# Kernel optimization log

Hardware: AMD Instinct MI355X
Metric: run time of the kernel (lower is better)

The kernel has to match this reference:

```python
import jax, jax.numpy as jnp
import numpy as np

NUM_HEADS = 8
NUM_CLS = 1
WINDOW = 4          # one-sided window radius
DILATION = 2
THETA = 10000.0
COORD_HIGH = 100000.0


def _rotate_half(t):
    # [..., x1, x2, ...] -> [..., -x2, x1, ...]
    x1 = t[..., 0::2]
    x2 = t[..., 1::2]
    return jnp.stack([-x2, x1], axis=-1).reshape(t.shape)


def _rope2d(t, coords):
    # t: (B, H, L, D), coords: (B, L, 2)
    head_dim = t.shape[-1]
    half = head_dim // 2
    inv_freq = 1.0 / (THETA ** (jnp.arange(0, half, 2, dtype=jnp.float32) / half))  # (half//2,)
    xy = coords.astype(jnp.float32) / COORD_HIGH                                    # (B, L, 2)
    fx = xy[..., 0][..., None] * inv_freq                                           # (B, L, half//2)
    fy = xy[..., 1][..., None] * inv_freq
    fx = jnp.repeat(fx, 2, axis=-1)                                                 # (B, L, half)
    fy = jnp.repeat(fy, 2, axis=-1)
    freqs = jnp.concatenate([fx, fy], axis=-1)                                      # (B, L, D)
    cos = jnp.cos(freqs)[:, None]                                                   # (B, 1, L, D)
    sin = jnp.sin(freqs)[:, None]
    return t * cos + _rotate_half(t) * sin


def setup_inputs() -> dict:
    key = jax.random.key(0)
    k1, k2, k3, k4 = jax.random.split(key, 4)
    B, L, E = 2, 8192, 512
    S = NUM_CLS + L
    x = jax.random.normal(k1, (B, S, E), dtype=jnp.float32)
    coords = jax.random.randint(k2, (B, L, 2), 0, 100000, dtype=jnp.int32)
    w_qkv = jax.random.normal(k3, (3 * E, E), dtype=jnp.float32) * 0.02
    b_qkv = jnp.zeros((3 * E,), dtype=jnp.float32)
    w_out = jax.random.normal(k4, (E, E), dtype=jnp.float32) * 0.02
    b_out = jnp.zeros((E,), dtype=jnp.float32)
    return {"x": x, "coords": coords, "w_qkv": w_qkv, "b_qkv": b_qkv,
            "w_out": w_out, "b_out": b_out}


def reference(x, coords, w_qkv, b_qkv, w_out, b_out):
    B, S, E = x.shape
    H = NUM_HEADS
    D = E // H
    L = S - NUM_CLS
    scale = 1.0 / np.sqrt(D).astype(np.float32)

    qkv = x @ w_qkv.T + b_qkv                                  # (B, S, 3E)
    qkv = qkv.reshape(B, S, 3, H, D).transpose(2, 0, 3, 1, 4)  # (3, B, H, S, D)
    q, k, v = qkv[0], qkv[1], qkv[2]

    # 2D RoPE on patch tokens only
    q = jnp.concatenate([q[:, :, :NUM_CLS], _rope2d(q[:, :, NUM_CLS:], coords)], axis=2)
    k = jnp.concatenate([k[:, :, :NUM_CLS], _rope2d(k[:, :, NUM_CLS:], coords)], axis=2)

    # ---- global CLS queries attend to all tokens ----
    s_cls = jnp.einsum('bhqd,bhkd->bhqk', q[:, :, :NUM_CLS], k) * scale
    cls_out = jnp.einsum('bhqk,bhkd->bhqd', jax.nn.softmax(s_cls, axis=-1), v)

    # ---- patch queries: CLS keys + dilated local window ----
    q_p = q[:, :, NUM_CLS:]
    k_p, v_p = k[:, :, NUM_CLS:], v[:, :, NUM_CLS:]
    k_cls, v_cls = k[:, :, :NUM_CLS], v[:, :, :NUM_CLS]

    pad = WINDOW * DILATION
    W = 2 * WINDOW + 1
    kp = jnp.pad(k_p, ((0, 0), (0, 0), (pad, pad), (0, 0)))
    vp = jnp.pad(v_p, ((0, 0), (0, 0), (pad, pad), (0, 0)))

    pos = jnp.arange(L)
    offsets = jnp.arange(W) * DILATION
    gidx = pos[:, None] + offsets[None, :]                     # (L, W), indices into padded seq
    kw = jnp.take(kp, gidx, axis=2)                            # (B, H, L, W, D)
    vw = jnp.take(vp, gidx, axis=2)

    win_pos = (jnp.arange(W) - WINDOW) * DILATION
    in_bounds = (pos[:, None] + win_pos >= 0) & (pos[:, None] + win_pos < L)  # (L, W)

    s_win = jnp.einsum('bhld,bhlwd->bhlw', q_p, kw) * scale
    s_win = jnp.where(in_bounds, s_win, -jnp.inf)
    s_c = jnp.einsum('bhld,bhcd->bhlc', q_p, k_cls) * scale
    attn = jax.nn.softmax(jnp.concatenate([s_c, s_win], axis=-1), axis=-1)  # (B,H,L,C+W)

    patch_out = (jnp.einsum('bhlc,bhcd->bhld', attn[..., :NUM_CLS], v_cls)
                 + jnp.einsum('bhlw,bhlwd->bhld', attn[..., NUM_CLS:], vw))

    out = jnp.concatenate([cls_out, patch_out], axis=2)        # (B, H, S, D)
    out = out.transpose(0, 2, 1, 3).reshape(B, S, E)
    return out @ w_out.T + b_out
```

## Files before the change

kernel.cpp:

```cpp
#include <hip/hip_runtime.h>
#include <math.h>

#define B_ 2
#define S_ 8193
#define L_ 8192
#define E_ 512
#define H_ 8
#define D_ 64
#define QKV_COLS 1536
#define SCALE 0.125f
#define M_ROWS 16386
#define M_PAD 16512

typedef unsigned short u16;
typedef __attribute__((ext_vector_type(8))) short bf16x8;
typedef __attribute__((ext_vector_type(8))) unsigned short u16x8;
typedef __attribute__((ext_vector_type(4))) float f32x4;

__device__ __forceinline__ u16 f2bf(float f) {
    unsigned u = __float_as_uint(f);
    unsigned r = (u + 0x7fffu + ((u >> 16) & 1u)) >> 16;
    return (u16)r;
}
__device__ __forceinline__ float bf2f(u16 h) {
    return __uint_as_float((unsigned)h << 16);
}

__device__ __forceinline__ void gload_lds16(const void* g, void* l) {
    __builtin_amdgcn_global_load_lds(
        (const __attribute__((address_space(1))) void*)g,
        (__attribute__((address_space(3))) void*)l, 16, 0, 0);
}

#define WAITV8() asm volatile("s_waitcnt vmcnt(8)" ::: "memory")
#define WAITV4() asm volatile("s_waitcnt vmcnt(4)" ::: "memory")
#define WAITV0() asm volatile("s_waitcnt vmcnt(0)" ::: "memory")
#define LGKM0()  asm volatile("s_waitcnt lgkmcnt(0)" ::: "memory")
#define BAR()    __builtin_amdgcn_s_barrier()

#define PREP_W1 (QKV_COLS * E_ / 4)
#define PREP_W2 (E_ * E_ / 4)
#define PREP_W3 (B_ * L_ * 32)
#define PREP_W4 ((M_PAD - M_ROWS) * E_ / 8)
#define PREP_TOTAL (PREP_W1 + PREP_W2 + PREP_W3 + PREP_W4)

__global__ __launch_bounds__(256) void prep_kernel(
    const float* __restrict__ w_qkv, const float* __restrict__ w_out,
    const int* __restrict__ coords,
    u16* __restrict__ wqb, u16* __restrict__ wob,
    float2* __restrict__ tab, u16* __restrict__ attnb)
{
    long i = (long)blockIdx.x * 256 + threadIdx.x;
    if (i < PREP_W1) {
        const float4 v = *(const float4*)(w_qkv + i * 4);
        ushort4 o = { f2bf(v.x), f2bf(v.y), f2bf(v.z), f2bf(v.w) };
        *(ushort4*)(wqb + i * 4) = o;
        return;
    }
    i -= PREP_W1;
    if (i < PREP_W2) {
        const float4 v = *(const float4*)(w_out + i * 4);
        ushort4 o = { f2bf(v.x), f2bf(v.y), f2bf(v.z), f2bf(v.w) };
        *(ushort4*)(wob + i * 4) = o;
        return;
    }
    i -= PREP_W2;
    if (i < PREP_W3) {
        const int p2 = (int)i & 31;
        const int bl = (int)i >> 5;
        const float coord = (float)coords[(size_t)bl * 2 + (p2 >> 4)] * 1e-5f;
        const float inv = exp2f(-0.83048202372184f * (float)(p2 & 15));
        float sn, cs;
        __sincosf(coord * inv, &sn, &cs);
        tab[i] = make_float2(cs, sn);
        return;
    }
    i -= PREP_W3;
    if (i < PREP_W4) {
        u16x8 z = {};
        *(u16x8*)(attnb + (size_t)M_ROWS * E_ + i * 8) = z;
    }
}

__global__ __launch_bounds__(512, 4) void gemm_qkv_fused(
    const float* __restrict__ X, const u16* __restrict__ W,
    const float* __restrict__ bias, u16* __restrict__ C,
    const float2* __restrict__ tab, int M, int N, int K)
{
    __shared__ __align__(16) u16 smem[16384];

    const int nwg = gridDim.x * gridDim.y;
    const int orig = blockIdx.y * gridDim.x + blockIdx.x;
    const int qq = nwg >> 3, rr = nwg & 7;
    const int xcd = orig & 7, off = orig >> 3;
    const int wgid = (xcd < rr ? xcd * (qq + 1) : rr * (qq + 1) + (xcd - rr) * qq) + off;
    const int m0 = (wgid / gridDim.x) * 128;
    const int n0 = (wgid % gridDim.x) * 128;

    const int tid  = threadIdx.x;
    const int wid  = tid >> 6;
    const int lane = tid & 63;
    const int wm = (wid >> 2) * 64;
    const int wn = (wid & 3) * 32;
    const int fr = lane & 15;
    const int fq = lane >> 4;

    const int r0 = tid >> 3;
    const int c8 = tid & 7;
    const int aoff0 = r0 * 32 + (((c8 >> 1) ^ (r0 & 3)) * 8) + (c8 & 1) * 4;

    const int wrow = tid >> 2;
    const int wch  = (tid & 3) ^ (wrow & 3);

    float4 ra[2];
    f32x4 acc[4][2] = {};

    #define ALOAD(k0)                                                           \
        do {                                                                    \
            _Pragma("unroll")                                                   \
            for (int i = 0; i < 2; ++i) {                                       \
                const int gm = m0 + r0 + 64 * i;                                \
                ra[i] = (gm < M)                                                \
                    ? *(const float4*)(X + (size_t)gm * K + (k0) + c8 * 4)      \
                    : make_float4(0.f, 0.f, 0.f, 0.f);                          \
            }                                                                   \
        } while (0)

    #define ADSW(buf)                                                           \
        do {                                                                    \
            u16* as_ = smem + (buf) * 4096;                                     \
            _Pragma("unroll")                                                   \
            for (int i = 0; i < 2; ++i) {                                       \
                ushort4 o;                                                      \
                o.x = f2bf(ra[i].x); o.y = f2bf(ra[i].y);                       \
                o.z = f2bf(ra[i].z); o.w = f2bf(ra[i].w);                       \
                *(ushort4*)(as_ + aoff0 + 2048 * i) = o;                        \
            }                                                                   \
        } while (0)

    #define WSTAGE(buf, k0)                                                     \
        gload_lds16(W + (size_t)(n0 + wrow) * K + (k0) + wch * 8,               \
                    smem + 8192 + (buf) * 4096 + wid * 512)

    #define COMPUTE(buf)                                                         \
        do {                                                                     \
            const u16* as_ = smem + (buf) * 4096;                                \
            const u16* bs_ = smem + 8192 + (buf) * 4096;                         \
            bf16x8 a[4], b[2];                                                   \
            _Pragma("unroll")                                                    \
            for (int mi = 0; mi < 4; ++mi) {                                     \
                const int r_ = wm + mi * 16 + fr;                                \
                a[mi] = *(const bf16x8*)(as_ + r_ * 32 + ((fq ^ (r_ & 3)) * 8)); \
            }                                                                    \
            _Pragma("unroll")                                                    \
            for (int ni = 0; ni < 2; ++ni) {                                     \
                const int r_ = wn + ni * 16 + fr;                                \
                b[ni] = *(const bf16x8*)(bs_ + r_ * 32 + ((fq ^ (r_ & 3)) * 8)); \
            }                                                                    \
            _Pragma("unroll")                                                    \
            for (int mi = 0; mi < 4; ++mi)                                       \
                _Pragma("unroll")                                                \
                for (int ni = 0; ni < 2; ++ni)                                   \
                    acc[mi][ni] = __builtin_amdgcn_mfma_f32_16x16x32_bf16(       \
                        a[mi], b[ni], acc[mi][ni], 0, 0, 0);                     \
        } while (0)

    const int nt = K / 32;

    ALOAD(0); WSTAGE(0, 0);
    WAITV0();
    ADSW(0);
    ALOAD(32); WSTAGE(1, 32);
    LGKM0(); BAR();

    for (int t = 0; t < nt; ++t) {
        COMPUTE(t & 1);
        if (t + 1 < nt) {
            WAITV0();
            ADSW((t + 1) & 1);
            if (t + 2 < nt) ALOAD((t + 2) * 32);
            LGKM0(); BAR();
            if (t + 2 < nt) WSTAGE(t & 1, (t + 2) * 32);
        }
    }

    #undef ALOAD
    #undef ADSW
    #undef WSTAGE
    #undef COMPUTE

    __syncthreads();

    u16* st = smem;
    const bool rope_blk = (n0 < 2 * E_);
    #pragma unroll
    for (int mi = 0; mi < 4; ++mi) {
        #pragma unroll
        for (int j = 0; j < 4; ++j) {
            const int row = wm + mi * 16 + fq * 4 + j;
            const int gm = m0 + row;
            int b = 0, s = gm;
            if (gm >= S_) { b = 1; s = gm - S_; }
            const bool rot = rope_blk && (gm < M) && (s > 0);
            const float2* trow = tab + ((size_t)(b * L_ + (s - 1)) << 5);
            #pragma unroll
            for (int ni = 0; ni < 2; ++ni) {
                const int col = wn + ni * 16 + fr;
                const int gn = n0 + col;
                float v = acc[mi][ni][j] + bias[gn];
                const float partner = __shfl_xor(v, 1, 64);
                if (rot) {
                    const float2 tt = trow[(gn & 63) >> 1];
                    v = (gn & 1) ? (v * tt.x + partner * tt.y)
                                 : (v * tt.x - partner * tt.y);
                }
                st[row * 128 + col] = f2bf(v);
            }
        }
    }
    __syncthreads();
    #pragma unroll
    for (int i = 0; i < 4; ++i) {
        const int slot = i * 512 + tid;
        const int row = slot >> 4;
        const int coff = (slot & 15) * 8;
        const int gm = m0 + row;
        if (gm < M)
            *(u16x8*)(C + (size_t)gm * N + n0 + coff) =
                *(const u16x8*)(st + row * 128 + coff);
    }
}

__global__ __launch_bounds__(256) void gemm_out_128(
    const u16* __restrict__ A, const u16* __restrict__ W,
    const float* __restrict__ bias, float* __restrict__ C,
    int M, int N, int K)
{
    __shared__ __align__(16) u16 smem[32768];

    const int nwg = gridDim.x * gridDim.y;
    const int orig = blockIdx.y * gridDim.x + blockIdx.x;
    const int qq = nwg >> 3, rr = nwg & 7;
    const int xcd = orig & 7, off = orig >> 3;
    const int wgid = (xcd < rr ? xcd * (qq + 1) : rr * (qq + 1) + (xcd - rr) * qq) + off;
    const int m0 = (wgid / gridDim.x) * 128;
    const int n0 = (wgid % gridDim.x) * 128;

    const int tid  = threadIdx.x;
    const int wid  = tid >> 6;
    const int lane = tid & 63;
    const int wm = (wid >> 1) * 64;
    const int wn = (wid & 1) * 64;

    const int srow = lane >> 2;
    const int scol = ((lane & 3) ^ ((lane >> 3) & 3)) * 8;
    const int fr = lane & 15;
    const int fq = lane >> 4;
    const int sfq = (fq ^ ((fr >> 1) & 3)) * 8;

    const int c0 = wid * 2, c1 = wid * 2 + 1;
    const u16* ga0 = A + (size_t)(m0 + c0 * 16 + srow) * K + scol;
    const u16* ga1 = A + (size_t)(m0 + c1 * 16 + srow) * K + scol;
    const u16* gb0 = W + (size_t)(n0 + c0 * 16 + srow) * K + scol;
    const u16* gb1 = W + (size_t)(n0 + c1 * 16 + srow) * K + scol;
    const int la0 = c0 * 16 * 32, la1 = c1 * 16 * 32;

    f32x4 acc[4][4] = {};

    #define STAGE(bi, k0)                                       \
        do {                                                    \
            u16* as_ = smem + (bi) * 4096;                      \
            u16* bs_ = smem + 16384 + (bi) * 4096;              \
            gload_lds16(ga0 + (k0), as_ + la0);                 \
            gload_lds16(ga1 + (k0), as_ + la1);                 \
            gload_lds16(gb0 + (k0), bs_ + la0);                 \
            gload_lds16(gb1 + (k0), bs_ + la1);                 \
        } while (0)

    #define COMPUTE(bi)                                                          \
        do {                                                                     \
            const u16* as_ = smem + (bi) * 4096;                                 \
            const u16* bs_ = smem + 16384 + (bi) * 4096;                         \
            bf16x8 a[4], b[4];                                                   \
            _Pragma("unroll")                                                    \
            for (int mi = 0; mi < 4; ++mi)                                       \
                a[mi] = *(const bf16x8*)(as_ + (wm + mi * 16 + fr) * 32 + sfq);  \
            _Pragma("unroll")                                                    \
            for (int ni = 0; ni < 4; ++ni)                                       \
                b[ni] = *(const bf16x8*)(bs_ + (wn + ni * 16 + fr) * 32 + sfq);  \
            _Pragma("unroll")                                                    \
            for (int mi = 0; mi < 4; ++mi)                                       \
                _Pragma("unroll")                                                \
                for (int ni = 0; ni < 4; ++ni)                                   \
                    acc[mi][ni] = __builtin_amdgcn_mfma_f32_16x16x32_bf16(       \
                        a[mi], b[ni], acc[mi][ni], 0, 0, 0);                     \
        } while (0)

    const int nt = K / 32;

    STAGE(0, 0);
    STAGE(1, 32);
    STAGE(2, 64);

    int t = 0;
    for (; t <= nt - 4; ++t) {
        WAITV8(); BAR();
        COMPUTE(t & 3);
        STAGE((t + 3) & 3, (t + 3) * 32);
    }
    WAITV8(); BAR(); COMPUTE(t & 3); ++t;
    WAITV4(); BAR(); COMPUTE(t & 3); ++t;
    WAITV0(); BAR(); COMPUTE(t & 3);

    #undef STAGE
    #undef COMPUTE

    __syncthreads();

    float* stf = (float*)smem;
    #pragma unroll
    for (int mi = 0; mi < 4; ++mi)
        #pragma unroll
        for (int j = 0; j < 4; ++j) {
            const int r = wm + mi * 16 + fq * 4 + j;
            #pragma unroll
            for (int ni = 0; ni < 4; ++ni) {
                const int c = wn + ni * 16 + fr;
                stf[r * 128 + c] = acc[mi][ni][j] + bias[n0 + c];
            }
        }
    __syncthreads();
    #pragma unroll
    for (int i = 0; i < 16; ++i) {
        const int ch = i * 256 + tid;
        const int row = ch >> 5;
        const int coff = (ch & 31) * 4;
        const int gm = m0 + row;
        if (gm < M)
            *(float4*)(C + (size_t)gm * N + n0 + coff) =
                *(const float4*)(stf + row * 128 + coff);
    }
}

#define NCHUNK 64
#define CLS_ROWS 129
#define CLS_BLOCKS (B_ * H_ * NCHUNK)
#define PQT 256
#define PATCH_BLOCKS (B_ * H_ * (L_ / PQT))

__global__ __launch_bounds__(256) void attn_fused(
    const u16* __restrict__ qkvb, float* __restrict__ part,
    u16* __restrict__ attnb)
{
    __shared__ __align__(16) u16 sbuf[272 * 64];
    __shared__ float kcvc[128];
    __shared__ float sm4[4], sl4[4];

    const int blk = blockIdx.x;

    if (blk < CLS_BLOCKS) {
        const int bh = blk >> 6, ch = blk & 63;
        const int b = bh >> 3, h = bh & 7;
        const int wid = threadIdx.x >> 6, lane = threadIdx.x & 63;
        const size_t base = (size_t)b * S_ * QKV_COLS;

        const float q = bf2f(qkvb[base + h * D_ + lane]);

        const int lo = ch * CLS_ROWS;
        const int hi = (lo + CLS_ROWS < S_) ? lo + CLS_ROWS : S_;

        float m = -1e30f, lsum = 0.f, acc = 0.f;
        for (int j = lo + wid; j < hi; j += 4) {
            const size_t roff = base + (size_t)j * QKV_COLS;
            float t = q * bf2f(qkvb[roff + E_ + h * D_ + lane]);
            #pragma unroll
            for (int o = 32; o; o >>= 1) t += __shfl_xor(t, o, 64);
            t *= SCALE;
            const float mn = fmaxf(m, t);
            const float corr = __expf(m - mn);
            const float p = __expf(t - mn);
            lsum = lsum * corr + p;
            acc = acc * corr + p * bf2f(qkvb[roff + 2 * E_ + h * D_ + lane]);
            m = mn;
        }

        float* sacc = (float*)sbuf;
        if (lane == 0) { sm4[wid] = m; sl4[wid] = lsum; }
        sacc[wid * 64 + lane] = acc;
        __syncthreads();
        if (wid == 0) {
            const float gm = fmaxf(fmaxf(sm4[0], sm4[1]), fmaxf(sm4[2], sm4[3]));
            float gl = 0.f, ga = 0.f;
            #pragma unroll
            for (int w = 0; w < 4; ++w) {
                const float c = __expf(sm4[w] - gm);
                gl += sl4[w] * c;
                ga += sacc[w * 64 + lane] * c;
            }
            float* pp = part + ((size_t)bh * NCHUNK + ch) * 66;
            if (lane == 0) { pp[0] = gm; pp[1] = gl; }
            pp[2 + lane] = ga;
        }
        return;
    }

    const int pblk = blk - CLS_BLOCKS;
    const int qt = pblk & 31;
    const int h = (pblk >> 5) & 7;
    const int b = pblk >> 8;
    const int l0 = qt * PQT;
    const size_t base = (size_t)b * S_ * QKV_COLS;
    const int hoff = h * D_;

    u16* kv = sbuf;
    float* kc = kcvc;
    float* vc = kcvc + 64;

    const int t = threadIdx.x;

    if (t < 64) kc[t] = bf2f(qkvb[base + E_ + hoff + t]);
    else if (t < 128) vc[t - 64] = bf2f(qkvb[base + 2 * E_ + hoff + (t - 64)]);

    #pragma unroll
    for (int i = 0; i < 9; ++i) {
        const int s = i * 256 + t;
        if (s < 272 * 8) {
            const int r = s >> 3, c = s & 7;
            const int lg = l0 - 8 + r;
            u16x8 v = {};
            if (lg >= 0 && lg < L_)
                v = *(const u16x8*)(qkvb + base + (size_t)(1 + lg) * QKV_COLS + E_ + hoff + c * 8);
            *(u16x8*)(kv + r * 64 + ((c ^ (r & 7)) * 8)) = v;
        }
    }
    __syncthreads();

    const int l = l0 + t;
    const size_t qrow = base + (size_t)(1 + l) * QKV_COLS + hoff;

    float s[10];
    #pragma unroll
    for (int w = 0; w < 10; ++w) s[w] = 0.f;

    #pragma unroll
    for (int c = 0; c < 8; ++c) {
        const u16x8 qv = *(const u16x8*)(qkvb + qrow + c * 8);
        float qf[8];
        #pragma unroll
        for (int i = 0; i < 8; ++i) qf[i] = bf2f(qv[i]);
        #pragma unroll
        for (int i = 0; i < 8; ++i) s[0] += qf[i] * kc[c * 8 + i];
        #pragma unroll
        for (int w = 0; w < 9; ++w) {
            const int kr = t + 2 * w;
            const u16x8 kk = *(const u16x8*)(kv + kr * 64 + ((c ^ (kr & 7)) * 8));
            #pragma unroll
            for (int i = 0; i < 8; ++i) s[1 + w] += qf[i] * bf2f(kk[i]);
        }
    }

    s[0] *= SCALE;
    #pragma unroll
    for (int w = 0; w < 9; ++w) {
        const int lp = l + 2 * w - 8;
        s[1 + w] = (lp >= 0 && lp < L_) ? s[1 + w] * SCALE : -1e30f;
    }
    float m = s[0];
    #pragma unroll
    for (int w = 1; w < 10; ++w) m = fmaxf(m, s[w]);
    float sum = 0.f;
    #pragma unroll
    for (int w = 0; w < 10; ++w) { s[w] = __expf(s[w] - m); sum += s[w]; }
    const float rsum = 1.0f / sum;

    __syncthreads();
    #pragma unroll
    for (int i = 0; i < 9; ++i) {
        const int sl = i * 256 + t;
        if (sl < 272 * 8) {
            const int r = sl >> 3, c = sl & 7;
            const int lg = l0 - 8 + r;
            u16x8 v = {};
            if (lg >= 0 && lg < L_)
                v = *(const u16x8*)(qkvb + base + (size_t)(1 + lg) * QKV_COLS + 2 * E_ + hoff + c * 8);
            *(u16x8*)(kv + r * 64 + ((c ^ (r & 7)) * 8)) = v;
        }
    }
    __syncthreads();

    const size_t orow = (size_t)(b * S_ + 1 + l) * E_ + hoff;
    #pragma unroll
    for (int c = 0; c < 8; ++c) {
        float acc[8];
        #pragma unroll
        for (int i = 0; i < 8; ++i) acc[i] = s[0] * vc[c * 8 + i];
        #pragma unroll
        for (int w = 0; w < 9; ++w) {
            const int vr = t + 2 * w;
            const u16x8 vv = *(const u16x8*)(kv + vr * 64 + ((c ^ (vr & 7)) * 8));
            #pragma unroll
            for (int i = 0; i < 8; ++i) acc[i] += s[1 + w] * bf2f(vv[i]);
        }
        u16x8 o;
        #pragma unroll
        for (int i = 0; i < 8; ++i) o[i] = f2bf(acc[i] * rsum);
        *(u16x8*)(attnb + orow + c * 8) = o;
    }
}

__global__ __launch_bounds__(64) void cls_attn_stage2(
    const float* __restrict__ part, u16* __restrict__ attnb)
{
    const int bh = blockIdx.x;
    const int lane = threadIdx.x;
    const int b = bh >> 3, h = bh & 7;
    float gm = -1e30f;
    for (int c = 0; c < NCHUNK; ++c)
        gm = fmaxf(gm, part[((size_t)bh * NCHUNK + c) * 66]);
    float gl = 0.f, ga = 0.f;
    for (int c = 0; c < NCHUNK; ++c) {
        const float* pp = part + ((size_t)bh * NCHUNK + c) * 66;
        const float w = __expf(pp[0] - gm);
        gl += pp[1] * w;
        ga += pp[2 + lane] * w;
    }
    attnb[(size_t)(b * S_) * E_ + h * D_ + lane] = f2bf(ga / gl);
}

extern "C" void kernel_launch(void* const* d_in, const int* in_sizes, int n_in,
                              void* d_out, int out_size, void* d_ws, size_t ws_size,
                              hipStream_t stream)
{
    const float* x      = (const float*)d_in[0];
    const int*   coords = (const int*)  d_in[1];
    const float* w_qkv  = (const float*)d_in[2];
    const float* b_qkv  = (const float*)d_in[3];
    const float* w_out  = (const float*)d_in[4];
    const float* b_out  = (const float*)d_in[5];
    float* out = (float*)d_out;

    u16*   qkvb  = (u16*)d_ws;
    u16*   attnb = qkvb + (size_t)M_ROWS * QKV_COLS;
    u16*   wqb   = attnb + (size_t)M_PAD * E_;
    u16*   wob   = wqb + (size_t)QKV_COLS * E_;
    float* part  = (float*)(wob + (size_t)E_ * E_);
    float2* tab  = (float2*)(part + (size_t)16 * NCHUNK * 66);

    prep_kernel<<<(PREP_TOTAL + 255) / 256, 256, 0, stream>>>(
        w_qkv, w_out, coords, wqb, wob, tab, attnb);

    {
        dim3 grid(QKV_COLS / 128, M_PAD / 128);
        gemm_qkv_fused<<<grid, 512, 0, stream>>>(
            x, wqb, b_qkv, qkvb, tab, M_ROWS, QKV_COLS, E_);
    }

    attn_fused<<<CLS_BLOCKS + PATCH_BLOCKS, 256, 0, stream>>>(qkvb, part, attnb);

    cls_attn_stage2<<<B_ * H_, 64, 0, stream>>>(part, attnb);

    {
        dim3 grid(E_ / 128, M_PAD / 128);
        gemm_out_128<<<grid, 256, 0, stream>>>(
            attnb, wob, b_out, out, M_ROWS, E_, E_);
    }
}
```

Before: 143.0 us.

## Pre-convert x to bf16 and unify both GEMMs into one templated kernel

The prep kernel now converts the fp32 input x to a padded bf16 buffer, so the QKV GEMM can stage both operands directly into LDS with async global-to-LDS loads instead of doing register loads and fp32-to-bf16 conversion inside the main loop. Both GEMMs now share one 512-thread templated kernel with a simple double-buffered pipeline and launch bounds of 6 waves per SIMD. The output GEMM moves from a 256-thread, 4-stage kernel to this shared design, with a two-pass epilogue that stages half the tile at a time. This costs an extra write and read of x in bf16. The output projection also loses its deeper prefetch pipeline.

```diff
diff --git a/kernel.cpp b/kernel.cpp
--- a/kernel.cpp
+++ b/kernel.cpp
@@ -32,25 +32,35 @@
         (__attribute__((address_space(3))) void*)l, 16, 0, 0);
 }
 
-#define WAITV8() asm volatile("s_waitcnt vmcnt(8)" ::: "memory")
-#define WAITV4() asm volatile("s_waitcnt vmcnt(4)" ::: "memory")
 #define WAITV0() asm volatile("s_waitcnt vmcnt(0)" ::: "memory")
-#define LGKM0()  asm volatile("s_waitcnt lgkmcnt(0)" ::: "memory")
 #define BAR()    __builtin_amdgcn_s_barrier()
 
+#define PREP_W0 (M_PAD * E_ / 4)
 #define PREP_W1 (QKV_COLS * E_ / 4)
 #define PREP_W2 (E_ * E_ / 4)
 #define PREP_W3 (B_ * L_ * 32)
 #define PREP_W4 ((M_PAD - M_ROWS) * E_ / 8)
-#define PREP_TOTAL (PREP_W1 + PREP_W2 + PREP_W3 + PREP_W4)
+#define PREP_TOTAL (PREP_W0 + PREP_W1 + PREP_W2 + PREP_W3 + PREP_W4)
 
 __global__ __launch_bounds__(256) void prep_kernel(
+    const float* __restrict__ x,
     const float* __restrict__ w_qkv, const float* __restrict__ w_out,
     const int* __restrict__ coords,
-    u16* __restrict__ wqb, u16* __restrict__ wob,
+    u16* __restrict__ xb, u16* __restrict__ wqb, u16* __restrict__ wob,
     float2* __restrict__ tab, u16* __restrict__ attnb)
 {
     long i = (long)blockIdx.x * 256 + threadIdx.x;
+    if (i < PREP_W0) {
+        const long row = i >> 7;
+        ushort4 o = make_ushort4(0, 0, 0, 0);
+        if (row < M_ROWS) {
+            const float4 v = *(const float4*)(x + i * 4);
+            o.x = f2bf(v.x); o.y = f2bf(v.y); o.z = f2bf(v.z); o.w = f2bf(v.w);
+        }
+        *(ushort4*)(xb + i * 4) = o;
+        return;
+    }
+    i -= PREP_W0;
     if (i < PREP_W1) {
         const float4 v = *(const float4*)(w_qkv + i * 4);
         ushort4 o = { f2bf(v.x), f2bf(v.y), f2bf(v.z), f2bf(v.w) };
@@ -82,10 +92,11 @@
     }
 }
 
-__global__ __launch_bounds__(512, 4) void gemm_qkv_fused(
-    const float* __restrict__ X, const u16* __restrict__ W,
-    const float* __restrict__ bias, u16* __restrict__ C,
-    const float2* __restrict__ tab, int M, int N, int K)
+template <int MODE>
+__global__ __launch_bounds__(512, 6) void gemm512(
+    const u16* __restrict__ A, const u16* __restrict__ W,
+    const float* __restrict__ bias, void* __restrict__ Cv,
+    const float2* __restrict__ tab, int M, int N)
 {
     __shared__ __align__(16) u16 smem[16384];
 
@@ -104,241 +115,125 @@
     const int wn = (wid & 3) * 32;
     const int fr = lane & 15;
     const int fq = lane >> 4;
-
-    const int r0 = tid >> 3;
-    const int c8 = tid & 7;
-    const int aoff0 = r0 * 32 + (((c8 >> 1) ^ (r0 & 3)) * 8) + (c8 & 1) * 4;
-
-    const int wrow = tid >> 2;
-    const int wch  = (tid & 3) ^ (wrow & 3);
-
-    float4 ra[2];
+    const int sfq = (fq ^ ((fr >> 1) & 3)) * 8;
+
+    const int arow = tid >> 2;
+    const int agch = ((tid & 3) ^ ((arow >> 1) & 3)) * 8;
+    const u16* ga = A + (size_t)(m0 + arow) * 512 + agch;
+    const u16* gw = W + (size_t)(n0 + arow) * 512 + agch;
+
     f32x4 acc[4][2] = {};
 
-    #define ALOAD(k0)                                                           \
+    #define STAGE(rb, kt)                                                       \
         do {                                                                    \
+            gload_lds16(ga + (kt) * 32, smem + (rb) * 4096 + wid * 512);        \
+            gload_lds16(gw + (kt) * 32, smem + 8192 + (rb) * 4096 + wid * 512); \
+        } while (0)
+
+    #define COMPUTE(rb)                                                         \
+        do {                                                                    \
+            const u16* as_ = smem + (rb) * 4096;                                \
+            const u16* bs_ = smem + 8192 + (rb) * 4096;                         \
+            bf16x8 a[4], b[2];                                                  \
             _Pragma("unroll")                                                   \
-            for (int i = 0; i < 2; ++i) {                                       \
-                const int gm = m0 + r0 + 64 * i;                                \
-                ra[i] = (gm < M)                                                \
-                    ? *(const float4*)(X + (size_t)gm * K + (k0) + c8 * 4)      \
-                    : make_float4(0.f, 0.f, 0.f, 0.f);                          \
-            }                                                                   \
+            for (int mi = 0; mi < 4; ++mi)                                      \
+                a[mi] = *(const bf16x8*)(as_ + (wm + mi * 16 + fr) * 32 + sfq); \
+            _Pragma("unroll")                                                   \
+            for (int ni = 0; ni < 2; ++ni)                                      \
+                b[ni] = *(const bf16x8*)(bs_ + (wn + ni * 16 + fr) * 32 + sfq); \
+            _Pragma("unroll")                                                   \
+            for (int mi = 0; mi < 4; ++mi)                                      \
+                _Pragma("unroll")                                               \
+                for (int ni = 0; ni < 2; ++ni)                                  \
+                    acc[mi][ni] = __builtin_amdgcn_mfma_f32_16x16x32_bf16(      \
+                        a[mi], b[ni], acc[mi][ni], 0, 0, 0);                    \
         } while (0)
 
-    #define ADSW(buf)                                                           \
-        do {                                                                    \
-            u16* as_ = smem + (buf) * 4096;                                     \
-            _Pragma("unroll")                                                   \
-            for (int i = 0; i < 2; ++i) {                                       \
-                ushort4 o;                                                      \
-                o.x = f2bf(ra[i].x); o.y = f2bf(ra[i].y);                       \
-                o.z = f2bf(ra[i].z); o.w = f2bf(ra[i].w);                       \
-                *(ushort4*)(as_ + aoff0 + 2048 * i) = o;                        \
-            }                                                                   \
-        } while (0)
-
-    #define WSTAGE(buf, k0)                                                     \
-        gload_lds16(W + (size_t)(n0 + wrow) * K + (k0) + wch * 8,               \
-                    smem + 8192 + (buf) * 4096 + wid * 512)
-
-    #define COMPUTE(buf)                                                         \
-        do {                                                                     \
-            const u16* as_ = smem + (buf) * 4096;                                \
-            const u16* bs_ = smem + 8192 + (buf) * 4096;                         \
-            bf16x8 a[4], b[2];                                                   \
-            _Pragma("unroll")                                                    \
-            for (int mi = 0; mi < 4; ++mi) {                                     \
-                const int r_ = wm + mi * 16 + fr;                                \
-                a[mi] = *(const bf16x8*)(as_ + r_ * 32 + ((fq ^ (r_ & 3)) * 8)); \
-            }                                                                    \
-            _Pragma("unroll")                                                    \
-            for (int ni = 0; ni < 2; ++ni) {                                     \
-                const int r_ = wn + ni * 16 + fr;                                \
-                b[ni] = *(const bf16x8*)(bs_ + r_ * 32 + ((fq ^ (r_ & 3)) * 8)); \
-            }                                                                    \
-            _Pragma("unroll")                                                    \
-            for (int mi = 0; mi < 4; ++mi)                                       \
-                _Pragma("unroll")                                                \
-                for (int ni = 0; ni < 2; ++ni)                                   \
-                    acc[mi][ni] = __builtin_amdgcn_mfma_f32_16x16x32_bf16(       \
-                        a[mi], b[ni], acc[mi][ni], 0, 0, 0);                     \
-        } while (0)
-
-    const int nt = K / 32;
-
-    ALOAD(0); WSTAGE(0, 0);
-    WAITV0();
-    ADSW(0);
-    ALOAD(32); WSTAGE(1, 32);
-    LGKM0(); BAR();
-
-    for (int t = 0; t < nt; ++t) {
+    STAGE(0, 0);
+
+    for (int t = 0; t < 16; ++t) {
+        WAITV0();
+        BAR();
+        if (t + 1 < 16) STAGE((t + 1) & 1, t + 1);
         COMPUTE(t & 1);
-        if (t + 1 < nt) {
-            WAITV0();
-            ADSW((t + 1) & 1);
-            if (t + 2 < nt) ALOAD((t + 2) * 32);
-            LGKM0(); BAR();
-            if (t + 2 < nt) WSTAGE(t & 1, (t + 2) * 32);
-        }
-    }
-
-    #undef ALOAD
-    #undef ADSW
-    #undef WSTAGE
-    #undef COMPUTE
-
-    __syncthreads();
-
-    u16* st = smem;
-    const bool rope_blk = (n0 < 2 * E_);
-    #pragma unroll
-    for (int mi = 0; mi < 4; ++mi) {
-        #pragma unroll
-        for (int j = 0; j < 4; ++j) {
-            const int row = wm + mi * 16 + fq * 4 + j;
-            const int gm = m0 + row;
-            int b = 0, s = gm;
-            if (gm >= S_) { b = 1; s = gm - S_; }
-            const bool rot = rope_blk && (gm < M) && (s > 0);
-            const float2* trow = tab + ((size_t)(b * L_ + (s - 1)) << 5);
-            #pragma unroll
-            for (int ni = 0; ni < 2; ++ni) {
-                const int col = wn + ni * 16 + fr;
-                const int gn = n0 + col;
-                float v = acc[mi][ni][j] + bias[gn];
-                const float partner = __shfl_xor(v, 1, 64);
-                if (rot) {
-                    const float2 tt = trow[(gn & 63) >> 1];
-                    v = (gn & 1) ? (v * tt.x + partner * tt.y)
-                                 : (v * tt.x - partner * tt.y);
-                }
-                st[row * 128 + col] = f2bf(v);
-            }
-        }
-    }
-    __syncthreads();
-    #pragma unroll
-    for (int i = 0; i < 4; ++i) {
-        const int slot = i * 512 + tid;
-        const int row = slot >> 4;
-        const int coff = (slot & 15) * 8;
-        const int gm = m0 + row;
-        if (gm < M)
-            *(u16x8*)(C + (size_t)gm * N + n0 + coff) =
-                *(const u16x8*)(st + row * 128 + coff);
-    }
-}
-
-__global__ __launch_bounds__(256) void gemm_out_128(
-    const u16* __restrict__ A, const u16* __restrict__ W,
-    const float* __restrict__ bias, float* __restrict__ C,
-    int M, int N, int K)
-{
-    __shared__ __align__(16) u16 smem[32768];
-
-    const int nwg = gridDim.x * gridDim.y;
-    const int orig = blockIdx.y * gridDim.x + blockIdx.x;
-    const int qq = nwg >> 3, rr = nwg & 7;
-    const int xcd = orig & 7, off = orig >> 3;
-    const int wgid = (xcd < rr ? xcd * (qq + 1) : rr * (qq + 1) + (xcd - rr) * qq) + off;
-    const int m0 = (wgid / gridDim.x) * 128;
-    const int n0 = (wgid % gridDim.x) * 128;
-
-    const int tid  = threadIdx.x;
-    const int wid  = tid >> 6;
-    const int lane = tid & 63;
-    const int wm = (wid >> 1) * 64;
-    const int wn = (wid & 1) * 64;
-
-    const int srow = lane >> 2;
-    const int scol = ((lane & 3) ^ ((lane >> 3) & 3)) * 8;
-    const int fr = lane & 15;
-    const int fq = lane >> 4;
-    const int sfq = (fq ^ ((fr >> 1) & 3)) * 8;
-
-    const int c0 = wid * 2, c1 = wid * 2 + 1;
-    const u16* ga0 = A + (size_t)(m0 + c0 * 16 + srow) * K + scol;
-    const u16* ga1 = A + (size_t)(m0 + c1 * 16 + srow) * K + scol;
-    const u16* gb0 = W + (size_t)(n0 + c0 * 16 + srow) * K + scol;
-    const u16* gb1 = W + (size_t)(n0 + c1 * 16 + srow) * K + scol;
-    const int la0 = c0 * 16 * 32, la1 = c1 * 16 * 32;
-
-    f32x4 acc[4][4] = {};
-
-    #define STAGE(bi, k0)                                       \
-        do {                                                    \
-            u16* as_ = smem + (bi) * 4096;                      \
-            u16* bs_ = smem + 16384 + (bi) * 4096;              \
-            gload_lds16(ga0 + (k0), as_ + la0);                 \
-            gload_lds16(ga1 + (k0), as_ + la1);                 \
-            gload_lds16(gb0 + (k0), bs_ + la0);                 \
-            gload_lds16(gb1 + (k0), bs_ + la1);                 \
-        } while (0)
-
-    #define COMPUTE(bi)                                                          \
-        do {                                                                     \
-            const u16* as_ = smem + (bi) * 4096;                                 \
-            const u16* bs_ = smem + 16384 + (bi) * 4096;                         \
-            bf16x8 a[4], b[4];                                                   \
-            _Pragma("unroll")                                                    \
-            for (int mi = 0; mi < 4; ++mi)                                       \
-                a[mi] = *(const bf16x8*)(as_ + (wm + mi * 16 + fr) * 32 + sfq);  \
-            _Pragma("unroll")                                                    \
-            for (int ni = 0; ni < 4; ++ni)                                       \
-                b[ni] = *(const bf16x8*)(bs_ + (wn + ni * 16 + fr) * 32 + sfq);  \
-            _Pragma("unroll")                                                    \
-            for (int mi = 0; mi < 4; ++mi)                                       \
-                _Pragma("unroll")                                                \
-                for (int ni = 0; ni < 4; ++ni)                                   \
-                    acc[mi][ni] = __builtin_amdgcn_mfma_f32_16x16x32_bf16(       \
-                        a[mi], b[ni], acc[mi][ni], 0, 0, 0);                     \
-        } while (0)
-
-    const int nt = K / 32;
-
-    STAGE(0, 0);
-    STAGE(1, 32);
-    STAGE(2, 64);
-
-    int t = 0;
-    for (; t <= nt - 4; ++t) {
-        WAITV8(); BAR();
-        COMPUTE(t & 3);
-        STAGE((t + 3) & 3, (t + 3) * 32);
-    }
-    WAITV8(); BAR(); COMPUTE(t & 3); ++t;
-    WAITV4(); BAR(); COMPUTE(t & 3); ++t;
-    WAITV0(); BAR(); COMPUTE(t & 3);
+    }
 
     #undef STAGE
     #undef COMPUTE
 
     __syncthreads();
 
-    float* stf = (float*)smem;
-    #pragma unroll
-    for (int mi = 0; mi < 4; ++mi)
-        #pragma unroll
-        for (int j = 0; j < 4; ++j) {
-            const int r = wm + mi * 16 + fq * 4 + j;
-            #pragma unroll
-            for (int ni = 0; ni < 4; ++ni) {
-                const int c = wn + ni * 16 + fr;
-                stf[r * 128 + c] = acc[mi][ni][j] + bias[n0 + c];
+    if (MODE == 1) {
+        u16* st = smem;
+        const bool rope_blk = (n0 < 2 * E_);
+        #pragma unroll
+        for (int mi = 0; mi < 4; ++mi) {
+            #pragma unroll
+            for (int j = 0; j < 4; ++j) {
+                const int row = wm + mi * 16 + fq * 4 + j;
+                const int gm = m0 + row;
+                int b = 0, s = gm;
+                if (gm >= S_) { b = 1; s = gm - S_; }
+                const bool rot = rope_blk && (gm < M) && (s > 0);
+                const float2* trow = tab + ((size_t)(b * L_ + (s - 1)) << 5);
+                #pragma unroll
+                for (int ni = 0; ni < 2; ++ni) {
+                    const int col = wn + ni * 16 + fr;
+                    const int gn = n0 + col;
+                    float v = acc[mi][ni][j] + bias[gn];
+                    const float partner = __shfl_xor(v, 1, 64);
+                    if (rot) {
+                        const float2 tt = trow[(gn & 63) >> 1];
+                        v = (gn & 1) ? (v * tt.x + partner * tt.y)
+                                     : (v * tt.x - partner * tt.y);
+                    }
+                    st[row * 128 + col] = f2bf(v);
+                }
             }
         }
-    __syncthreads();
-    #pragma unroll
-    for (int i = 0; i < 16; ++i) {
-        const int ch = i * 256 + tid;
-        const int row = ch >> 5;
-        const int coff = (ch & 31) * 4;
-        const int gm = m0 + row;
-        if (gm < M)
-            *(float4*)(C + (size_t)gm * N + n0 + coff) =
-                *(const float4*)(stf + row * 128 + coff);
+        __syncthreads();
+        u16* C = (u16*)Cv;
+        #pragma unroll
+        for (int i = 0; i < 4; ++i) {
+            const int slot = i * 512 + tid;
+            const int row = slot >> 4;
+            const int coff = (slot & 15) * 8;
+            const int gm = m0 + row;
+            if (gm < M)
+                *(u16x8*)(C + (size_t)gm * N + n0 + coff) =
+                    *(const u16x8*)(st + row * 128 + coff);
+        }
+    } else {
+        float* stf = (float*)smem;
+        float* C = (float*)Cv;
+        #pragma unroll
+        for (int h = 0; h < 2; ++h) {
+            if ((wid >> 2) == h) {
+                #pragma unroll
+                for (int mi = 0; mi < 4; ++mi)
+                    #pragma unroll
+                    for (int j = 0; j < 4; ++j) {
+                        const int lrow = mi * 16 + fq * 4 + j;
+                        #pragma unroll
+                        for (int ni = 0; ni < 2; ++ni) {
+                            const int col = wn + ni * 16 + fr;
+                            stf[lrow * 128 + col] = acc[mi][ni][j] + bias[n0 + col];
+                        }
+                    }
+            }
+            __syncthreads();
+            #pragma unroll
+            for (int i = 0; i < 4; ++i) {
+                const int slot = i * 512 + tid;
+                const int row = slot >> 5;
+                const int coff = (slot & 31) * 4;
+                const int gm = m0 + h * 64 + row;
+                if (gm < M)
+                    *(float4*)(C + (size_t)gm * N + n0 + coff) =
+                        *(const float4*)(stf + row * 128 + coff);
+            }
+            __syncthreads();
+        }
     }
 }
 
@@ -541,18 +436,19 @@
 
     u16*   qkvb  = (u16*)d_ws;
     u16*   attnb = qkvb + (size_t)M_ROWS * QKV_COLS;
-    u16*   wqb   = attnb + (size_t)M_PAD * E_;
+    u16*   xb    = attnb + (size_t)M_PAD * E_;
+    u16*   wqb   = xb + (size_t)M_PAD * E_;
     u16*   wob   = wqb + (size_t)QKV_COLS * E_;
     float* part  = (float*)(wob + (size_t)E_ * E_);
     float2* tab  = (float2*)(part + (size_t)16 * NCHUNK * 66);
 
     prep_kernel<<<(PREP_TOTAL + 255) / 256, 256, 0, stream>>>(
-        w_qkv, w_out, coords, wqb, wob, tab, attnb);
+        x, w_qkv, w_out, coords, xb, wqb, wob, tab, attnb);
 
     {
         dim3 grid(QKV_COLS / 128, M_PAD / 128);
-        gemm_qkv_fused<<<grid, 512, 0, stream>>>(
-            x, wqb, b_qkv, qkvb, tab, M_ROWS, QKV_COLS, E_);
+        gemm512<1><<<grid, 512, 0, stream>>>(
+            xb, wqb, b_qkv, qkvb, tab, M_ROWS, QKV_COLS);
     }
 
     attn_fused<<<CLS_BLOCKS + PATCH_BLOCKS, 256, 0, stream>>>(qkvb, part, attnb);
@@ -561,7 +457,7 @@
 
     {
         dim3 grid(E_ / 128, M_PAD / 128);
-        gemm_out_128<<<grid, 256, 0, stream>>>(
-            attnb, wob, b_out, out, M_ROWS, E_, E_);
-    }
-}
+        gemm512<0><<<grid, 512, 0, stream>>>(
+            attnb, wob, b_out, out, nullptr, M_ROWS, E_);
+    }
+}
```

Result: faster. 135.1 us (-5.5%).
